# Kernel optimization log

Hardware: AMD Instinct MI355X
Metric: run time of the kernel (lower is better)

Reference implementation:

```python
import jax, jax.numpy as jnp
import numpy as np

DIM = 768
HEADS = 8

def setup_inputs() -> dict:
    key = jax.random.key(0)
    k1, k2, k3, k4 = jax.random.split(key, 4)
    x = jax.random.normal(k1, (4, 2048, DIM), dtype=jnp.float32)
    # torch Linear(D, 3D, bias=False): weight [3D, D]; store transposed [D, 3D]
    W_qkv = jax.random.normal(k2, (DIM, 3 * DIM), dtype=jnp.float32) * (DIM ** -0.5)
    W_o = jax.random.normal(k3, (DIM, DIM), dtype=jnp.float32) * (DIM ** -0.5)
    b_o = jax.random.normal(k4, (DIM,), dtype=jnp.float32) * 0.01
    return {"x": x, "W_qkv": W_qkv, "W_o": W_o, "b_o": b_o}

def reference(x, W_qkv, W_o, b_o):
    B, N, D = x.shape
    H = HEADS
    dh = D // H
    scale = dh ** -0.5
    qkv = x @ W_qkv                                   # [B, N, 3D]
    qkv = qkv.reshape(B, N, 3, H, dh)
    qkv = jnp.transpose(qkv, (2, 0, 3, 1, 4))         # [3, B, H, N, dh]
    Q, K, V = qkv[0], qkv[1], qkv[2]
    scores = jnp.einsum('bhqd,bhkd->bhqk', Q, K) * scale  # [B, H, N, N]
    attn = jax.nn.softmax(scores, axis=-1)
    out = jnp.einsum('bhqk,bhkd->bhqd', attn, V)      # [B, H, N, dh]
    # Faithful to original: reshape [B,H,N,dh] -> [B,N,D] WITHOUT head transpose
    out = out.reshape(B, N, D)
    return out @ W_o + b_o
```

## Files before the change

kernel.cpp:

```cpp
#include <hip/hip_runtime.h>

typedef __attribute__((ext_vector_type(8))) short short8;
typedef __attribute__((ext_vector_type(4))) float f32x4;
typedef __attribute__((ext_vector_type(4))) _Float16 half4;
typedef __attribute__((ext_vector_type(8))) _Float16 half8;
typedef __attribute__((ext_vector_type(2))) __fp16 fp16x2;

#define B_SZ 4
#define NSEQ 2048
#define DIM  768
#define NH   8
#define DH   96

__device__ __forceinline__ unsigned short f2bf(float f) {
  unsigned int u = __float_as_uint(f);
  u += 0x7fffu + ((u >> 16) & 1u);
  return (unsigned short)(u >> 16);
}

__device__ __forceinline__ float fexp2(float x) {
#if __has_builtin(__builtin_amdgcn_exp2f)
  return __builtin_amdgcn_exp2f(x);
#else
  return exp2f(x);
#endif
}

__device__ __forceinline__ void glds16(const void* g, void* l) {
  __builtin_amdgcn_global_load_lds((const __attribute__((address_space(1))) void*)g,
                                   (__attribute__((address_space(3))) void*)l, 16, 0, 0);
}

__global__ __launch_bounds__(256) void cvt_x_kernel(const float* __restrict__ x,
                                                    unsigned short* __restrict__ xb) {
  int i = blockIdx.x * 256 + threadIdx.x;
  float4 v = ((const float4*)x)[i];
  ushort4 o;
  o.x = f2bf(v.x); o.y = f2bf(v.y); o.z = f2bf(v.z); o.w = f2bf(v.w);
  ((ushort4*)xb)[i] = o;
}

__global__ __launch_bounds__(256) void transpose_cvt_kernel(const float* __restrict__ W,
                                                            unsigned short* __restrict__ WT,
                                                            int ncols) {
  __shared__ float tile[32][33];
  int tx = threadIdx.x, ty = threadIdx.y;
  int c0 = blockIdx.x * 32;
  int r0 = blockIdx.y * 32;
#pragma unroll
  for (int i = 0; i < 4; i++)
    tile[ty + i * 8][tx] = W[(size_t)(r0 + ty + i * 8) * ncols + c0 + tx];
  __syncthreads();
#pragma unroll
  for (int i = 0; i < 4; i++)
    WT[(size_t)(c0 + ty + i * 8) * 768 + r0 + tx] = f2bf(tile[tx][ty + i * 8]);
}

template <int EPI>
__global__ __launch_bounds__(256) void gemm_bt(
    const unsigned short* __restrict__ A, const unsigned short* __restrict__ Bt,
    unsigned short* __restrict__ qo, unsigned short* __restrict__ ko,
    _Float16* __restrict__ vo, float* __restrict__ fo,
    const float* __restrict__ bias)
{
  __shared__ unsigned short As[128 * 32];
  __shared__ unsigned short Bs[128 * 32];
  const int t = threadIdx.x;
  const int w = t >> 6, lane = t & 63;
  const int l15 = lane & 15, qd = lane >> 4;
  const int asw = (l15 >> 1) & 3;
  const int m0 = blockIdx.y * 128, n0 = blockIdx.x * 128;
  const int wm = (w >> 1) * 64, wn = (w & 1) * 64;

  const int sr = lane >> 2;
  const int sc = ((lane & 3) ^ ((sr >> 1) & 3)) * 8;
  const unsigned short* ga = A  + (size_t)(m0 + w * 16 + sr) * DIM + sc;
  const unsigned short* gb = Bt + (size_t)(n0 + w * 16 + sr) * DIM + sc;

  f32x4 acc[4][4] = {};

  for (int k0 = 0; k0 < DIM; k0 += 32) {
    glds16(ga + k0,            &As[w * 512]);
    glds16(ga + 64 * DIM + k0, &As[(4 + w) * 512]);
    glds16(gb + k0,            &Bs[w * 512]);
    glds16(gb + 64 * DIM + k0, &Bs[(4 + w) * 512]);
    __syncthreads();
    short8 af[4], bfr[4];
#pragma unroll
    for (int i = 0; i < 4; i++)
      af[i]  = *(const short8*)&As[(wm + i * 16 + l15) * 32 + (qd ^ asw) * 8];
#pragma unroll
    for (int i = 0; i < 4; i++)
      bfr[i] = *(const short8*)&Bs[(wn + i * 16 + l15) * 32 + (qd ^ asw) * 8];
#pragma unroll
    for (int mi = 0; mi < 4; mi++)
#pragma unroll
      for (int ni = 0; ni < 4; ni++)
        acc[mi][ni] = __builtin_amdgcn_mfma_f32_16x16x32_bf16(af[mi], bfr[ni], acc[mi][ni], 0, 0, 0);
    __syncthreads();
  }

#pragma unroll
  for (int mi = 0; mi < 4; mi++)
#pragma unroll
    for (int ni = 0; ni < 4; ni++) {
      int rowb = m0 + wm + mi * 16 + qd * 4;
      int col  = n0 + wn + ni * 16 + l15;
      if (EPI == 0) {
        int b = rowb >> 11, n = rowb & 2047;
        int s = col / DIM;
        int rem = col - s * DIM;
        int hh = rem / DH;
        int c = rem - hh * DH;
        size_t bh = (size_t)(b * NH + hh);
        if (s == 2) {
          half4 pk;
#pragma unroll
          for (int r = 0; r < 4; r++) pk[r] = (_Float16)acc[mi][ni][r];
          *(half4*)&vo[(bh * DH + c) * NSEQ + n] = pk;
        } else if (s == 0) {
#pragma unroll
          for (int r = 0; r < 4; r++)
            qo[(bh * NSEQ + n + r) * DH + c] = f2bf(acc[mi][ni][r] * 0.1472444679f);
        } else {
#pragma unroll
          for (int r = 0; r < 4; r++)
            ko[(bh * NSEQ + n + r) * DH + c] = f2bf(acc[mi][ni][r]);
        }
      } else {
#pragma unroll
        for (int r = 0; r < 4; r++)
          fo[(size_t)(rowb + r) * DIM + col] = acc[mi][ni][r] + bias[col];
      }
    }
}

__global__ __launch_bounds__(256, 2) void flash_kernel(
    const unsigned short* __restrict__ Qb, const unsigned short* __restrict__ Kb,
    const _Float16* __restrict__ Vtb, unsigned short* __restrict__ Z)
{
  __shared__ unsigned char smem[24576];
  unsigned short* Qs = (unsigned short*)smem;
  unsigned short* Ks = (unsigned short*)smem;
  _Float16*       Vs = (_Float16*)(smem + 12288);

  const int t = threadIdx.x, w = t >> 6, lane = t & 63;
  const int l15 = lane & 15, qd = lane >> 4;
  const int swz = (l15 >> 1) & 3;
  const int vswz = l15 & 7;
  const int qt = blockIdx.x, h = blockIdx.y, b = blockIdx.z;
  const size_t bh = (size_t)(b * NH + h);
  const unsigned short* Qg = Qb + (bh * NSEQ + (size_t)qt * 128) * DH;
  const unsigned short* Kg = Kb + bh * NSEQ * DH;
  const _Float16*       Vg = Vtb + bh * (size_t)DH * NSEQ;

  int qoff[6];
#pragma unroll
  for (int i = 0; i < 6; i++) {
    int L = i * 256 + t;
    int r = L / 12, c = L - r * 12;
    qoff[i] = r * 96 + ((c ^ ((r >> 1) & 3)) * 8);
  }
  int koff[3];
#pragma unroll
  for (int i = 0; i < 3; i++) {
    int L = w * 192 + i * 64 + lane;
    int r = L / 12, c = L - r * 12;
    int fk = r >> 4, m = r & 15;
    int key = 32 * (fk & 1) + 4 * (fk >> 1) + 8 * (m >> 2) + (m & 3);
    koff[i] = key * 96 + ((c ^ ((r >> 1) & 3)) * 8);
  }
  int voff[3];
#pragma unroll
  for (int i = 0; i < 3; i++) {
    int L = i * 256 + t;
    int r = L >> 3, c = L & 7;
    voff[i] = r * NSEQ + ((c ^ (r & 7)) * 8);
  }

#pragma unroll
  for (int i = 0; i < 6; i++)
    glds16(Qg + qoff[i], &Qs[i * 2048 + w * 512]);
  __syncthreads();
  short8 qa[2][3];
#pragma unroll
  for (int fq = 0; fq < 2; fq++)
#pragma unroll
    for (int ks = 0; ks < 3; ks++)
      qa[fq][ks] = *(const short8*)&Qs[(w * 32 + fq * 16 + l15) * 96 + ((ks * 4 + qd) ^ swz) * 8];

  f32x4 o[2][7] = {};
  float mprev[2] = {-1e30f, -1e30f};
  const half8 onef = {(_Float16)1.f, (_Float16)1.f, (_Float16)1.f, (_Float16)1.f,
                      (_Float16)1.f, (_Float16)1.f, (_Float16)1.f, (_Float16)1.f};

  for (int kt = 0; kt < 32; kt++) {
    __syncthreads();
    const unsigned short* Kt = Kg + (size_t)kt * 64 * DH;
#pragma unroll
    for (int i = 0; i < 3; i++)
      glds16(Kt + koff[i], &Ks[w * 1536 + i * 512]);
    const _Float16* Vt = Vg + kt * 64;
#pragma unroll
    for (int i = 0; i < 3; i++)
      glds16(Vt + voff[i], &Vs[(i * 256 + w * 64) * 8]);
    __syncthreads();

    f32x4 s[2][4] = {};
#pragma unroll
    for (int ks = 0; ks < 3; ks++)
#pragma unroll
      for (int fk = 0; fk < 4; fk++) {
        short8 kf = *(const short8*)&Ks[(fk * 16 + l15) * 96 + ((ks * 4 + qd) ^ swz) * 8];
        s[0][fk] = __builtin_amdgcn_mfma_f32_16x16x32_bf16(kf, qa[0][ks], s[0][fk], 0, 0, 0);
        s[1][fk] = __builtin_amdgcn_mfma_f32_16x16x32_bf16(kf, qa[1][ks], s[1][fk], 0, 0, 0);
      }

#pragma unroll
    for (int fq = 0; fq < 2; fq++) {
      float mx = fmaxf(fmaxf(s[fq][0][0], s[fq][0][1]), fmaxf(s[fq][0][2], s[fq][0][3]));
#pragma unroll
      for (int fk = 1; fk < 4; fk++)
        mx = fmaxf(mx, fmaxf(fmaxf(s[fq][fk][0], s[fq][fk][1]), fmaxf(s[fq][fk][2], s[fq][fk][3])));
      mx = fmaxf(mx, __shfl_xor(mx, 16, 64));
      mx = fmaxf(mx, __shfl_xor(mx, 32, 64));
      float mnew = fmaxf(mprev[fq], mx);
      float alpha = fexp2(mprev[fq] - mnew);
      mprev[fq] = mnew;

      half4 pf[4];
#pragma unroll
      for (int fk = 0; fk < 4; fk++) {
        union { fp16x2 h2[2]; half4 h4; } u;
        u.h2[0] = __builtin_amdgcn_cvt_pkrtz(fexp2(s[fq][fk][0] - mnew), fexp2(s[fq][fk][1] - mnew));
        u.h2[1] = __builtin_amdgcn_cvt_pkrtz(fexp2(s[fq][fk][2] - mnew), fexp2(s[fq][fk][3] - mnew));
        pf[fk] = u.h4;
      }
#pragma unroll
      for (int i = 0; i < 7; i++) o[fq][i] = o[fq][i] * alpha;

#pragma unroll
      for (int p = 0; p < 2; p++) {
        union { half4 h4[2]; half8 h8; } bu;
        bu.h4[0] = pf[p]; bu.h4[1] = pf[p + 2];
#pragma unroll
        for (int fc = 0; fc < 6; fc++) {
          half8 vf = *(const half8*)&Vs[(fc * 16 + l15) * 64 + ((p * 4 + qd) ^ vswz) * 8];
          o[fq][fc] = __builtin_amdgcn_mfma_f32_16x16x32_f16(vf, bu.h8, o[fq][fc], 0, 0, 0);
        }
        o[fq][6] = __builtin_amdgcn_mfma_f32_16x16x32_f16(onef, bu.h8, o[fq][6], 0, 0, 0);
      }
    }
  }

#pragma unroll
  for (int fq = 0; fq < 2; fq++) {
    float inv = 1.0f / o[fq][6][0];
    int q = qt * 128 + w * 32 + fq * 16 + l15;
    size_t zbase = ((size_t)b * NSEQ + h * 256 + (q >> 3)) * DIM + (q & 7) * DH;
#pragma unroll
    for (int fc = 0; fc < 6; fc++)
#pragma unroll
      for (int r = 0; r < 4; r += 2) {
        unsigned int pkd = (unsigned int)f2bf(o[fq][fc][r] * inv)
                         | ((unsigned int)f2bf(o[fq][fc][r + 1] * inv) << 16);
        *(unsigned int*)&Z[zbase + fc * 16 + qd * 4 + r] = pkd;
      }
  }
}

extern "C" void kernel_launch(void* const* d_in, const int* in_sizes, int n_in,
                              void* d_out, int out_size, void* d_ws, size_t ws_size,
                              hipStream_t stream)
{
  (void)in_sizes; (void)n_in; (void)out_size; (void)ws_size;
  const float* x    = (const float*)d_in[0];
  const float* Wqkv = (const float*)d_in[1];
  const float* Wo   = (const float*)d_in[2];
  const float* bo   = (const float*)d_in[3];
  float* out = (float*)d_out;

  unsigned short* ws    = (unsigned short*)d_ws;
  unsigned short* xb    = ws;
  unsigned short* wqkvT = xb    + (size_t)8192 * 768;
  unsigned short* woT   = wqkvT + (size_t)2304 * 768;
  unsigned short* Qw    = woT   + (size_t)768 * 768;
  unsigned short* Kw    = Qw    + (size_t)6291456;
  _Float16*       Vw    = (_Float16*)(Kw + (size_t)6291456);
  unsigned short* Zw    = (unsigned short*)(Vw + (size_t)6291456);

  cvt_x_kernel<<<6144, 256, 0, stream>>>(x, xb);
  transpose_cvt_kernel<<<dim3(72, 24), dim3(32, 8), 0, stream>>>(Wqkv, wqkvT, 2304);
  transpose_cvt_kernel<<<dim3(24, 24), dim3(32, 8), 0, stream>>>(Wo, woT, 768);
  gemm_bt<0><<<dim3(18, 64), 256, 0, stream>>>(xb, wqkvT, Qw, Kw, Vw, nullptr, nullptr);
  flash_kernel<<<dim3(16, 8, 4), 256, 0, stream>>>(Qw, Kw, Vw, Zw);
  gemm_bt<1><<<dim3(6, 64), 256, 0, stream>>>(Zw, woT, nullptr, nullptr, nullptr, out, bo);
}
```

Baseline: 226.9 us.

## Double-buffer K/V tiles in flash attention and merge prep kernels into one launch

The flash attention loop now uses two LDS buffers for K and V. The load of tile kt+1 is issued before computing on tile kt, and the loop needs one barrier per iteration instead of two, so global-to-LDS transfers can overlap the MFMA and softmax work. The first tile is prefetched after the Q fragments are read, with an extra barrier because Q shares LDS with the first K buffer. LDS use per block doubles to 48KB, which could limit occupancy. Separately, the x conversion and the two weight transpose-convert kernels are folded into a single launch that dispatches on block index, removing two kernel launches.

After: 223.7 us. No clear change (-1.4%).

```diff
diff --git a/kernel.cpp b/kernel.cpp
--- a/kernel.cpp
+++ b/kernel.cpp
@@ -31,22 +31,26 @@
                                    (__attribute__((address_space(3))) void*)l, 16, 0, 0);
 }
 
-__global__ __launch_bounds__(256) void cvt_x_kernel(const float* __restrict__ x,
-                                                    unsigned short* __restrict__ xb) {
-  int i = blockIdx.x * 256 + threadIdx.x;
-  float4 v = ((const float4*)x)[i];
-  ushort4 o;
-  o.x = f2bf(v.x); o.y = f2bf(v.y); o.z = f2bf(v.z); o.w = f2bf(v.w);
-  ((ushort4*)xb)[i] = o;
-}
-
-__global__ __launch_bounds__(256) void transpose_cvt_kernel(const float* __restrict__ W,
-                                                            unsigned short* __restrict__ WT,
-                                                            int ncols) {
+__global__ __launch_bounds__(256) void prep_kernel(
+    const float* __restrict__ x, unsigned short* __restrict__ xb,
+    const float* __restrict__ Wqkv, unsigned short* __restrict__ wqkvT,
+    const float* __restrict__ Wo, unsigned short* __restrict__ woT)
+{
+  int blk = blockIdx.x;
+  if (blk < 6144) {
+    int i = blk * 256 + threadIdx.x;
+    float4 v = ((const float4*)x)[i];
+    ushort4 o;
+    o.x = f2bf(v.x); o.y = f2bf(v.y); o.z = f2bf(v.z); o.w = f2bf(v.w);
+    ((ushort4*)xb)[i] = o;
+    return;
+  }
   __shared__ float tile[32][33];
-  int tx = threadIdx.x, ty = threadIdx.y;
-  int c0 = blockIdx.x * 32;
-  int r0 = blockIdx.y * 32;
+  const float* W; unsigned short* WT; int ncols, bx, by;
+  if (blk < 7872) { int r = blk - 6144; W = Wqkv; WT = wqkvT; ncols = 2304; bx = r % 72; by = r / 72; }
+  else            { int r = blk - 7872; W = Wo;   WT = woT;   ncols = 768;  bx = r % 24; by = r / 24; }
+  int tx = threadIdx.x & 31, ty = threadIdx.x >> 5;
+  int c0 = bx * 32, r0 = by * 32;
 #pragma unroll
   for (int i = 0; i < 4; i++)
     tile[ty + i * 8][tx] = W[(size_t)(r0 + ty + i * 8) * ncols + c0 + tx];
@@ -139,10 +143,12 @@
     const unsigned short* __restrict__ Qb, const unsigned short* __restrict__ Kb,
     const _Float16* __restrict__ Vtb, unsigned short* __restrict__ Z)
 {
-  __shared__ unsigned char smem[24576];
-  unsigned short* Qs = (unsigned short*)smem;
-  unsigned short* Ks = (unsigned short*)smem;
-  _Float16*       Vs = (_Float16*)(smem + 12288);
+  __shared__ unsigned char smem[49152];
+  unsigned short* Qs  = (unsigned short*)smem;
+  unsigned short* Ks0 = (unsigned short*)smem;
+  _Float16*       Vs0 = (_Float16*)(smem + 12288);
+  unsigned short* Ks1 = (unsigned short*)(smem + 24576);
+  _Float16*       Vs1 = (_Float16*)(smem + 36864);
 
   const int t = threadIdx.x, w = t >> 6, lane = t & 63;
   const int l15 = lane & 15, qd = lane >> 4;
@@ -188,6 +194,14 @@
 #pragma unroll
     for (int ks = 0; ks < 3; ks++)
       qa[fq][ks] = *(const short8*)&Qs[(w * 32 + fq * 16 + l15) * 96 + ((ks * 4 + qd) ^ swz) * 8];
+  __syncthreads();
+
+#pragma unroll
+  for (int i = 0; i < 3; i++)
+    glds16(Kg + koff[i], &Ks0[w * 1536 + i * 512]);
+#pragma unroll
+  for (int i = 0; i < 3; i++)
+    glds16(Vg + voff[i], &Vs0[(i * 256 + w * 64) * 8]);
 
   f32x4 o[2][7] = {};
   float mprev[2] = {-1e30f, -1e30f};
@@ -196,15 +210,20 @@
 
   for (int kt = 0; kt < 32; kt++) {
     __syncthreads();
-    const unsigned short* Kt = Kg + (size_t)kt * 64 * DH;
-#pragma unroll
-    for (int i = 0; i < 3; i++)
-      glds16(Kt + koff[i], &Ks[w * 1536 + i * 512]);
-    const _Float16* Vt = Vg + kt * 64;
-#pragma unroll
-    for (int i = 0; i < 3; i++)
-      glds16(Vt + voff[i], &Vs[(i * 256 + w * 64) * 8]);
-    __syncthreads();
+    const unsigned short* Ks = (kt & 1) ? Ks1 : Ks0;
+    const _Float16*       Vs = (kt & 1) ? Vs1 : Vs0;
+    if (kt + 1 < 32) {
+      unsigned short* Ksn = (kt & 1) ? Ks0 : Ks1;
+      _Float16*       Vsn = (kt & 1) ? Vs0 : Vs1;
+      const unsigned short* Kt = Kg + (size_t)(kt + 1) * 64 * DH;
+      const _Float16*       Vt = Vg + (kt + 1) * 64;
+#pragma unroll
+      for (int i = 0; i < 3; i++)
+        glds16(Kt + koff[i], &Ksn[w * 1536 + i * 512]);
+#pragma unroll
+      for (int i = 0; i < 3; i++)
+        glds16(Vt + voff[i], &Vsn[(i * 256 + w * 64) * 8]);
+    }
 
     f32x4 s[2][4] = {};
 #pragma unroll
@@ -289,9 +308,7 @@
   _Float16*       Vw    = (_Float16*)(Kw + (size_t)6291456);
   unsigned short* Zw    = (unsigned short*)(Vw + (size_t)6291456);
 
-  cvt_x_kernel<<<6144, 256, 0, stream>>>(x, xb);
-  transpose_cvt_kernel<<<dim3(72, 24), dim3(32, 8), 0, stream>>>(Wqkv, wqkvT, 2304);
-  transpose_cvt_kernel<<<dim3(24, 24), dim3(32, 8), 0, stream>>>(Wo, woT, 768);
+  prep_kernel<<<8448, 256, 0, stream>>>(x, xb, Wqkv, wqkvT, Wo, woT);
   gemm_bt<0><<<dim3(18, 64), 256, 0, stream>>>(xb, wqkvT, Qw, Kw, Vw, nullptr, nullptr);
   flash_kernel<<<dim3(16, 8, 4), 256, 0, stream>>>(Qw, Kw, Vw, Zw);
   gemm_bt<1><<<dim3(6, 64), 256, 0, stream>>>(Zw, woT, nullptr, nullptr, nullptr, out, bo);
```
